# Kernel optimization log

Hardware: AMD Instinct MI355X
Metric: run time of the kernel (lower is better)

The kernel has to match this reference:

```python
import jax, jax.numpy as jnp
import numpy as np

EPS = 1e-5  # BatchNorm eps (inference mode, running_mean=0, running_var=1)

def conv3(x, w, b=None):
    y = jax.lax.conv_general_dilated(x, w, (1, 1), ((1, 1), (1, 1)),
                                     dimension_numbers=('NCHW', 'OIHW', 'NCHW'))
    if b is not None:
        y = y + b[None, :, None, None]
    return y

def bn(x, g):
    # g: [2, C] = (gamma, beta); eval-mode BN with running stats (0, 1)
    scale = (g[0] / jnp.sqrt(1.0 + EPS))[None, :, None, None]
    return x * scale + g[1][None, :, None, None]

def bcr(x, w, g, b=None):  # BasicConv2d: conv -> BN -> ReLU
    return jax.nn.relu(bn(conv3(x, w, b), g))

def setup_inputs() -> dict:
    key = jax.random.key(0)
    B, ch1, ch2, H, W = 2, 64, 128, 64, 64
    ks = jax.random.split(key, 16)
    w = lambda k, o, i: (jax.random.normal(k, (o, i, 3, 3), jnp.float32) * 0.05)
    g = lambda c: jnp.stack([jnp.ones((c,), jnp.float32), jnp.zeros((c,), jnp.float32)])
    return {
        'xs': jax.random.normal(ks[0], (B, ch1, H, W), jnp.float32),
        'xc': jax.random.normal(ks[1], (B, ch2, H, W), jnp.float32),
        'w_g1': w(ks[2], 32, ch1), 'g_g1': g(32),
        'w_g2': w(ks[3], 32, ch2), 'g_g2': g(32),
        'w_ls': w(ks[4], ch1, ch1 + 32), 'b_ls': jnp.zeros((ch1,), jnp.float32), 'g_ls': g(ch1),
        'w_lc': w(ks[5], ch2, ch2 + 32), 'b_lc': jnp.zeros((ch2,), jnp.float32), 'g_lc': g(ch2),
        'w_c1': w(ks[6], 32, ch1), 'g_c1': g(32),
        'w_c2': w(ks[7], 32, ch2), 'g_c2': g(32),
        'w_o1': w(ks[8], ch1, ch1), 'g_o1': g(ch1),
        'w_o2': w(ks[9], ch2, ch2), 'g_o2': g(ch2),
        'w_oa': w(ks[10], 1, 1), 'g_oa': g(1),
    }

def reference(xs, xc, w_g1, g_g1, w_g2, g_g2, w_ls, b_ls, g_ls,
              w_lc, b_lc, g_lc, w_c1, g_c1, w_c2, g_c2,
              w_o1, g_o1, w_o2, g_o2, w_oa, g_oa):
    B, ch1, H, W = xs.shape
    ch2 = xc.shape[1]
    N = H * W
    # global context: conv+BN+ReLU -> GAP (1x1) -> bilinear upsample from 1x1 == broadcast
    g_s = jnp.mean(bcr(xs, w_g1, g_g1), axis=(2, 3), keepdims=True)  # [B,32,1,1]
    g_c = jnp.mean(bcr(xc, w_g2, g_g2), axis=(2, 3), keepdims=True)
    gs = jnp.broadcast_to(g_s, (B, 32, H, W))
    gc = jnp.broadcast_to(g_c, (B, 32, H, W))
    xs1 = jax.nn.relu(bn(conv3(jnp.concatenate([gs, xs], axis=1), w_ls, b_ls), g_ls)) + xs
    xc1 = jax.nn.relu(bn(conv3(jnp.concatenate([gc, xc], axis=1), w_lc, b_lc), g_lc)) + xc
    # dual cross-spatial attention
    fs = bcr(xs1, w_c1, g_c1).reshape(B, 32, N)
    fc = bcr(xc1, w_c2, g_c2).reshape(B, 32, N)
    att = jnp.einsum('bcn,bcm->bnm', fs, fc)  # [B,N,N]
    sm_cols = jax.nn.softmax(att, axis=-2)    # softmax over n (rows)
    sm_rows = jax.nn.softmax(att, axis=-1)    # softmax over m
    outs = jnp.einsum('bcn,bnm->bcm', xs1.reshape(B, ch1, N), sm_cols).reshape(B, ch1, H, W)
    # xc_flat @ softmax(att^T, -2): (att^T).softmax(-2)[m,j] = sm_rows[j,m]
    outc = jnp.einsum('bcm,bjm->bcj', xc1.reshape(B, ch2, N), sm_rows).reshape(B, ch2, H, W)
    out_s = bcr(outs, w_o1, g_o1) + xs1
    out_c = bcr(outc, w_o2, g_o2) + xc1
    att2 = att + jnp.swapaxes(att, -1, -2)
    att3 = jax.nn.softmax(att2, axis=-2) + jnp.swapaxes(jax.nn.softmax(att2, axis=-1), -1, -2)
    att_map = bcr(att3[:, None], w_oa, g_oa)  # [B,1,N,N]
    return (att_map, out_s, out_c, g_s, g_c)
```

## Files before the change

### kernel.cpp

```cpp
#include <hip/hip_runtime.h>


#define LB __launch_bounds__(256)

constexpr float BN_SCALE = 0.99999500003749968f;
constexpr float NEG_BIG  = -3.402823466e38f;
constexpr float LOG2E    = 1.4426950408889634f;
constexpr float LN2      = 0.6931471805599453f;

typedef __attribute__((ext_vector_type(8))) short short8v;
typedef __attribute__((ext_vector_type(4))) float f32x4;

__device__ __forceinline__ ushort bf16rne(float f) {
    unsigned u = __float_as_uint(f);
    unsigned r = (u + 0x7FFFu + ((u >> 16) & 1u)) >> 16;
    return (ushort)r;
}

__device__ __forceinline__ void online_merge(float& mx, float& sm, float m2, float s2) {
    const float mn = fmaxf(mx, m2);
    sm = sm * __expf(mx - mn) + s2 * __expf(m2 - mn);
    mx = mn;
}

__global__ LB void transpose_bf(const float* __restrict__ in, ushort* __restrict__ outT,
                                int C, int HW)
{
    __shared__ float t[32][33];
    const int tid = threadIdx.x;
    const int tx = tid & 31, ty0 = tid >> 5;
    const int hw0 = blockIdx.x * 32, c0 = blockIdx.y * 32, b = blockIdx.z;
    #pragma unroll
    for (int i = 0; i < 4; ++i)
        t[ty0 + i * 8][tx] = in[((long)b * C + c0 + ty0 + i * 8) * HW + hw0 + tx];
    __syncthreads();
    #pragma unroll
    for (int i = 0; i < 4; ++i)
        outT[((long)b * HW + hw0 + ty0 + i * 8) * C + c0 + tx] =
            bf16rne(t[tx][ty0 + i * 8]);
}

template<int HASG, int OCB>
__global__ LB void conv3x3_mfma(
    const ushort* __restrict__ inT,
    const float* __restrict__ gconst,
    const float* __restrict__ w,
    const float* __restrict__ bias,
    const float* __restrict__ bn,
    const float* __restrict__ residual,
    float* __restrict__ out,
    ushort* __restrict__ outbf,
    ushort* __restrict__ outTbf,
    int Cg, int Cin, int Cout)
{
    constexpr int TILES = OCB / 16;
    constexpr int TPO = 256 / OCB;
    constexpr int J = 288 / TPO;
    __shared__ ushort ldsA[9][OCB][36];
    __shared__ float wg[OCB][10];
    const int tid = threadIdx.x;
    const int wv = tid >> 6, lane = tid & 63;
    const int fr = lane & 15, fg = lane >> 4;
    const int px0 = blockIdx.x * 64, ocb = blockIdx.y * OCB, b = blockIdx.z;
    const int Ct = Cg + Cin;
    const int p = px0 + wv * 16 + fr;
    const int y = p >> 6, x = p & 63;

    if (HASG) {
        for (int e = tid; e < OCB * 9; e += 256) {
            const int oc = e / 9, k = e % 9;
            float s = 0.f;
            for (int ic = 0; ic < Cg; ++ic)
                s += gconst[b * Cg + ic] * w[((long)(ocb + oc) * Ct + ic) * 9 + k];
            wg[oc][k] = s;
        }
    }

    int qv[9]; bool val[9];
    #pragma unroll
    for (int k = 0; k < 9; ++k) {
        const int yy = y + k / 3 - 1, xx = x + k % 3 - 1;
        val[k] = ((unsigned)yy < 64u) && ((unsigned)xx < 64u);
        qv[k] = val[k] ? (yy * 64 + xx) : 0;
    }

    f32x4 acc[TILES];
    #pragma unroll
    for (int t = 0; t < TILES; ++t) acc[t] = (f32x4){0.f, 0.f, 0.f, 0.f};
    const short8v bz = (short8v){0, 0, 0, 0, 0, 0, 0, 0};

    const int oc_st = tid / TPO, q = tid % TPO;
    const int base_ic = q * (J / 9);
    const ushort* inTb = inT + (long)b * 4096 * Cin + 8 * fg;

    const int NCH = Cin / 32;
    for (int c = 0; c < NCH; ++c) {
        __syncthreads();
        {
            const float* wp = w + (long)(ocb + oc_st) * Ct * 9
                              + (long)(Cg + c * 32) * 9 + q * J;
            #pragma unroll
            for (int j4 = 0; j4 < J; j4 += 4) {
                const float4 v4 = *(const float4*)&wp[j4];
                ldsA[(j4 + 0) % 9][oc_st][base_ic + (j4 + 0) / 9] = bf16rne(v4.x);
                ldsA[(j4 + 1) % 9][oc_st][base_ic + (j4 + 1) / 9] = bf16rne(v4.y);
                ldsA[(j4 + 2) % 9][oc_st][base_ic + (j4 + 2) / 9] = bf16rne(v4.z);
                ldsA[(j4 + 3) % 9][oc_st][base_ic + (j4 + 3) / 9] = bf16rne(v4.w);
            }
        }
        __syncthreads();
        const ushort* inc = inTb + c * 32;
        #pragma unroll
        for (int k = 0; k < 9; ++k) {
            const short8v bfrag = val[k] ? *(const short8v*)&inc[(long)qv[k] * Cin] : bz;
            #pragma unroll
            for (int t = 0; t < TILES; ++t) {
                const short8v afrag = *(const short8v*)&ldsA[k][t * 16 + fr][8 * fg];
                acc[t] = __builtin_amdgcn_mfma_f32_16x16x32_bf16(afrag, bfrag, acc[t], 0, 0, 0);
            }
        }
    }

    #pragma unroll
    for (int t = 0; t < TILES; ++t) {
        float v4[4];
        #pragma unroll
        for (int r = 0; r < 4; ++r) {
            const int ocl = t * 16 + fg * 4 + r;
            const int oc = ocb + ocl;
            float v = acc[t][r];
            if (bias) v += bias[oc];
            if (HASG) {
                #pragma unroll
                for (int k = 0; k < 9; ++k)
                    if (val[k]) v += wg[ocl][k];
            }
            v = fmaxf(fmaf(v, bn[oc] * BN_SCALE, bn[Cout + oc]), 0.f);
            const long oidx = ((long)(b * Cout + oc)) * 4096 + p;
            if (residual) v += residual[oidx];
            out[oidx] = v;
            if (outbf) outbf[oidx] = bf16rne(v);
            v4[r] = v;
        }
        if (outTbf) {
            ushort4 o;
            o.x = bf16rne(v4[0]); o.y = bf16rne(v4[1]);
            o.z = bf16rne(v4[2]); o.w = bf16rne(v4[3]);
            *(ushort4*)&outTbf[((long)(b * 4096 + p)) * Cout + ocb + t * 16 + fg * 4] = o;
        }
    }
}

__global__ LB void gap_kernel(const float* __restrict__ in,
                              float* __restrict__ o1, float* __restrict__ o2,
                              int C, int HW)
{
    const int c = blockIdx.x, b = blockIdx.y;
    const float* p = in + ((long)b * C + c) * HW;
    float s = 0.f;
    for (int i = threadIdx.x; i < HW; i += 256) s += p[i];
    #pragma unroll
    for (int off = 32; off; off >>= 1) s += __shfl_down(s, off);
    __shared__ float red[4];
    if ((threadIdx.x & 63) == 0) red[threadIdx.x >> 6] = s;
    __syncthreads();
    if (threadIdx.x == 0) {
        const float t = (red[0] + red[1] + red[2] + red[3]) / (float)HW;
        o1[b * C + c] = t;
        o2[b * C + c] = t;
    }
}

__global__ LB void att_gemm(const float* __restrict__ fs, const float* __restrict__ fc,
                            float* __restrict__ att, float* __restrict__ attT, int N)
{
    __shared__ float lfs[32][33];
    const int tid = threadIdx.x;
    const int m  = blockIdx.x * 256 + tid;
    const int n0 = blockIdx.y * 32;
    const int b  = blockIdx.z;
    for (int i = tid; i < 1024; i += 256) {
        const int c = i >> 5, nn = i & 31;
        lfs[c][nn] = fs[((long)b * 32 + c) * N + n0 + nn];
    }
    __syncthreads();
    float acc[32];
    #pragma unroll
    for (int i = 0; i < 32; ++i) acc[i] = 0.f;
    const float* fcp = fc + (long)b * 32 * N + m;
    #pragma unroll
    for (int c = 0; c < 32; ++c) {
        const float f = fcp[(long)c * N];
        #pragma unroll
        for (int nn = 0; nn < 32; ++nn) acc[nn] = fmaf(lfs[c][nn], f, acc[nn]);
    }
    float* op = att + ((long)b * N + n0) * N + m;
    #pragma unroll
    for (int nn = 0; nn < 32; ++nn) op[(long)nn * N] = acc[nn];
    float* opT = attT + ((long)b * N + m) * N + n0;
    #pragma unroll
    for (int q = 0; q < 8; ++q)
        *(float4*)&opT[q * 4] = make_float4(acc[q*4], acc[q*4+1], acc[q*4+2], acc[q*4+3]);
}

__global__ LB void tri_stats(const float* __restrict__ att, const float* __restrict__ attT,
                             float* __restrict__ McP, float* __restrict__ ScP,
                             float* __restrict__ MrP, float* __restrict__ SrP,
                             float* __restrict__ M2P, float* __restrict__ S2P, int N)
{
    __shared__ float lm[3][4][64], ls[3][4][64];
    const int c = threadIdx.x & 63, q = threadIdx.x >> 6;
    const int m = blockIdx.x * 64 + c;
    const int y = blockIdx.y, b = blockIdx.z;
    const long base = (long)b * N * N + ((long)y * 128 + q) * N + m;

    float av[32], tv[32];
    #pragma unroll
    for (int r = 0; r < 32; ++r) {
        const long off = base + (long)r * 4 * N;
        av[r] = att[off];
        tv[r] = attT[off];
    }
    float mc = av[0], mr = tv[0], m2 = av[0] + tv[0];
    #pragma unroll
    for (int r = 1; r < 32; ++r) {
        mc = fmaxf(mc, av[r]);
        mr = fmaxf(mr, tv[r]);
        m2 = fmaxf(m2, av[r] + tv[r]);
    }
    const float mcL = mc * LOG2E, mrL = mr * LOG2E, m2L = m2 * LOG2E;
    float sc = 0.f, sr = 0.f, s2 = 0.f;
    #pragma unroll
    for (int r = 0; r < 32; ++r) {
        sc += exp2f(fmaf(av[r], LOG2E, -mcL));
        sr += exp2f(fmaf(tv[r], LOG2E, -mrL));
        s2 += exp2f(fmaf(av[r] + tv[r], LOG2E, -m2L));
    }

    lm[0][q][c] = mc; ls[0][q][c] = sc;
    lm[1][q][c] = mr; ls[1][q][c] = sr;
    lm[2][q][c] = m2; ls[2][q][c] = s2;
    __syncthreads();
    if (q < 3) {
        float M = lm[q][0][c], S = ls[q][0][c];
        #pragma unroll
        for (int j = 1; j < 4; ++j) online_merge(M, S, lm[q][j][c], ls[q][j][c]);
        float* Pm = (q == 0) ? McP : ((q == 1) ? MrP : M2P);
        float* Ps = (q == 0) ? ScP : ((q == 1) ? SrP : S2P);
        Pm[((long)(b * 32 + y)) * N + m] = M;
        Ps[((long)(b * 32 + y)) * N + m] = S;
    }
}

__global__ LB void stats_comb32(const float* __restrict__ Mp, const float* __restrict__ Sp,
                                float* __restrict__ M, float* __restrict__ Sm,
                                float* __restrict__ C2L, int N)
{
    __shared__ float lm[4][64], ls[4][64];
    const int c = threadIdx.x & 63, q = threadIdx.x >> 6;
    const int n = blockIdx.x * 64 + c;
    const int b = blockIdx.y;
    float mx = NEG_BIG, sum = 0.f;
    #pragma unroll
    for (int j = 0; j < 8; ++j) {
        const int s = q * 8 + j;
        online_merge(mx, sum, Mp[((long)(b * 32 + s)) * N + n], Sp[((long)(b * 32 + s)) * N + n]);
    }
    lm[q][c] = mx; ls[q][c] = sum;
    __syncthreads();
    if (q == 0) {
        #pragma unroll
        for (int j = 1; j < 4; ++j) online_merge(mx, sum, lm[j][c], ls[j][c]);
        M[(long)b * N + n]  = mx;
        Sm[(long)b * N + n] = sum;
        if (C2L) C2L[(long)b * N + n] = (mx - LN2 + __logf(sum)) * LOG2E;
    }
}

template<int MROWS>
__global__ LB void sm_gemm_mfma(const ushort* __restrict__ Xbf,
                                const float* __restrict__ A,
                                const float* __restrict__ Mv,
                                float* __restrict__ p0, float* __restrict__ p1,
                                int N)
{
    constexpr int RT = MROWS / 32;
    constexpr int TPRA = 256 / MROWS;
    __shared__ ushort ldsA[MROWS][40];
    __shared__ ushort ldsB[32][40];

    const int tid = threadIdx.x;
    const int wave = tid >> 6, lane = tid & 63;
    const int col0 = blockIdx.x * 32;
    const int s = blockIdx.y, b = blockIdx.z;
    const int K0 = s * (N / 2);

    const int scol = tid >> 3, sq = tid & 7;
    const int ar = tid / TPRA;
    const int ak = (tid % TPRA) * (32 / TPRA);
    const int wct = wave & 1;
    const int wrh = wave >> 1;
    const int fr = lane & 15, fg = lane >> 4;

    f32x4 acc[RT];
    #pragma unroll
    for (int i = 0; i < RT; ++i) acc[i] = (f32x4){0.f, 0.f, 0.f, 0.f};

    const float* ab = A + ((long)b * N + col0) * N;
    const ushort* xb = Xbf + (long)b * MROWS * N;
    const float mvl = Mv[(long)b * N + col0 + scol] * LOG2E;

    for (int k0 = K0; k0 < K0 + N / 2; k0 += 32) {
        __syncthreads();
        #pragma unroll
        for (int j = 0; j < 32 / TPRA; j += 8) {
            const short8v av = *(const short8v*)&xb[(long)ar * N + k0 + ak + j];
            *(short8v*)&ldsA[ar][ak + j] = av;
        }
        const float4 v = *(const float4*)&ab[(long)scol * N + k0 + sq * 4];
        ushort4 bfv;
        bfv.x = bf16rne(exp2f(fmaf(v.x, LOG2E, -mvl)));
        bfv.y = bf16rne(exp2f(fmaf(v.y, LOG2E, -mvl)));
        bfv.z = bf16rne(exp2f(fmaf(v.z, LOG2E, -mvl)));
        bfv.w = bf16rne(exp2f(fmaf(v.w, LOG2E, -mvl)));
        *(ushort4*)&ldsB[scol][sq * 4] = bfv;
        __syncthreads();
        const short8v bfrag = *(const short8v*)&ldsB[wct * 16 + fr][8 * fg];
        #pragma unroll
        for (int rt = 0; rt < RT; ++rt) {
            const int row = wrh * (MROWS / 2) + rt * 16 + fr;
            const short8v afrag = *(const short8v*)&ldsA[row][8 * fg];
            acc[rt] = __builtin_amdgcn_mfma_f32_16x16x32_bf16(afrag, bfrag, acc[rt], 0, 0, 0);
        }
    }

    float* pp = (s == 0) ? p0 : p1;
    #pragma unroll
    for (int rt = 0; rt < RT; ++rt) {
        #pragma unroll
        for (int r = 0; r < 4; ++r) {
            const int row = wrh * (MROWS / 2) + rt * 16 + (lane >> 4) * 4 + r;
            const int col = col0 + wct * 16 + (lane & 15);
            pp[((long)b * MROWS + row) * N + col] = acc[rt][r];
        }
    }
}

template<int C>
__global__ LB void sm_reduce2(const float* __restrict__ p0, const float* __restrict__ p1,
                              const float* __restrict__ denom, float* __restrict__ outp, int N)
{
    const long idx = (long)blockIdx.x * 256 + threadIdx.x;
    const int m = (int)(idx & (long)(N - 1));
    const int b = (int)(idx / ((long)C * N));
    outp[idx] = (p0[idx] + p1[idx]) / denom[(long)b * N + m];
}

__global__ LB void attmap_conv(const float* __restrict__ att,
                               const float* __restrict__ attT,
                               const float* __restrict__ C2L,
                               const float* __restrict__ w, const float* __restrict__ g,
                               float* __restrict__ out, int N)
{
    __shared__ float tD[34][136];
    __shared__ float ldc[130];
    const int tid = threadIdx.x;
    const int x0 = (blockIdx.x & 31) * 128;
    const int y0 = (blockIdx.x >> 5) * 32;
    const int b = blockIdx.y;
    const float* ap = att + (long)b * N * N;
    const float* tp = attT + (long)b * N * N;
    const float* cp = C2L + (long)b * N;

    if (tid < 130) {
        const int xx = x0 + tid - 1;
        ldc[tid] = ((unsigned)xx < (unsigned)N) ? cp[xx] : 0.f;
    }
    __syncthreads();

    {
        const int xg = (tid & 31) * 4;
        const int rg = tid >> 5;
        #pragma unroll
        for (int i = 0; i < 5; ++i) {
            const int hy = rg + i * 8;
            if (hy < 34) {
                const int yy = y0 + hy - 1;
                float4 v = make_float4(0.f, 0.f, 0.f, 0.f);
                if ((unsigned)yy < (unsigned)N) {
                    const long off = (long)yy * N + x0 + xg;
                    const float4 a = *(const float4*)&ap[off];
                    const float4 t = *(const float4*)&tp[off];
                    v.x = exp2f(fmaf(a.x + t.x, LOG2E, -ldc[xg + 1]));
                    v.y = exp2f(fmaf(a.y + t.y, LOG2E, -ldc[xg + 2]));
                    v.z = exp2f(fmaf(a.z + t.z, LOG2E, -ldc[xg + 3]));
                    v.w = exp2f(fmaf(a.w + t.w, LOG2E, -ldc[xg + 4]));
                }
                *(float4*)&tD[hy][xg + 4] = v;
            }
        }
    }
    if (tid < 68) {
        const int c01 = tid & 1, hy = tid >> 1;
        const int col = c01 ? 132 : 3;
        const int xx = c01 ? (x0 + 128) : (x0 - 1);
        const int yy = y0 + hy - 1;
        float v = 0.f;
        if ((unsigned)yy < (unsigned)N && (unsigned)xx < (unsigned)N) {
            const long off = (long)yy * N + xx;
            v = exp2f(fmaf(ap[off] + tp[off], LOG2E, -ldc[c01 ? 129 : 0]));
        }
        tD[hy][col] = v;
    }
    __syncthreads();

    const float scale = g[0] * BN_SCALE, beta = g[1];
    const int tx2 = tid & 127, tyg = tid >> 7;
    float* ob = out + (long)b * N * N + (long)y0 * N + x0 + tx2;
    #pragma unroll
    for (int rr = 0; rr < 16; ++rr) {
        const int ly = tyg + rr * 2;
        float acc = 0.f;
        #pragma unroll
        for (int ky = 0; ky < 3; ++ky)
            #pragma unroll
            for (int kx = 0; kx < 3; ++kx)
                acc = fmaf(w[ky * 3 + kx], tD[ly + ky][tx2 + 3 + kx], acc);
        ob[(long)ly * N] = fmaxf(fmaf(acc, scale, beta), 0.f);
    }
}

extern "C" void kernel_launch(void* const* d_in, const int* in_sizes, int n_in,
                              void* d_out, int out_size, void* d_ws, size_t ws_size,
                              hipStream_t stream)
{
    const float* xs   = (const float*)d_in[0];
    const float* xc   = (const float*)d_in[1];
    const float* w_g1 = (const float*)d_in[2];
    const float* g_g1 = (const float*)d_in[3];
    const float* w_g2 = (const float*)d_in[4];
    const float* g_g2 = (const float*)d_in[5];
    const float* w_ls = (const float*)d_in[6];
    const float* b_ls = (const float*)d_in[7];
    const float* g_ls = (const float*)d_in[8];
    const float* w_lc = (const float*)d_in[9];
    const float* b_lc = (const float*)d_in[10];
    const float* g_lc = (const float*)d_in[11];
    const float* w_c1 = (const float*)d_in[12];
    const float* g_c1 = (const float*)d_in[13];
    const float* w_c2 = (const float*)d_in[14];
    const float* g_c2 = (const float*)d_in[15];
    const float* w_o1 = (const float*)d_in[16];
    const float* g_o1 = (const float*)d_in[17];
    const float* w_o2 = (const float*)d_in[18];
    const float* g_o2 = (const float*)d_in[19];
    const float* w_oa = (const float*)d_in[20];
    const float* g_oa = (const float*)d_in[21];

    const int B = 2, HW = 4096, N = 4096;

    float* ws = (float*)d_ws;
    float* xs1    = ws;
    float* xc1    = ws + 524288;
    float* fs     = ws + 1572864;
    float* fc     = ws + 1835008;
    float* t32    = ws + 2097152;
    float* McP    = ws + 1572864;
    float* ScP    = ws + 1835008;
    float* MrP    = ws + 2097152;
    float* SrP    = ws + 2359296;
    float* M2P    = ws + 2621440;
    float* S2P    = ws + 2883584;
    float* pg1    = ws + 1572864;
    float* outs_w = ws + 2359296;
    float* outc_w = ws + 2883584;
    float* gs_w   = ws + 3932160;
    float* gc_w   = ws + 3932224;
    float* Mc     = ws + 3932288;
    float* Sc     = ws + 3940480;
    float* Mr     = ws + 3948672;
    float* Sr     = ws + 3956864;
    float* M2     = ws + 3965056;
    float* S2     = ws + 3973248;
    float* C2L    = ws + 3981440;
    float* att    = ws + 4243584;
    float* attT   = ws + 37798016;

    float* out = (float*)d_out;
    float* out_attmap = out;
    ushort* xs1bf   = (ushort*)out;
    ushort* xc1bf   = (ushort*)(out + 262144);
    ushort* xcT     = (ushort*)(out + 786432);
    ushort* outcT   = (ushort*)(out + 786432);
    ushort* xsT     = (ushort*)(out + 1310720);
    ushort* outs_wT = (ushort*)(out + 1310720);
    ushort* xs1T    = (ushort*)(out + 1572864);
    ushort* xc1T    = (ushort*)(out + 1835008);
    float* out_s      = out + 33554432;
    float* out_c      = out + 34078720;
    float* out_gs     = out + 35127296;
    float* out_gc     = out + 35127360;
    float* pg0        = out + 33554432;

    const dim3 blk(256);

    transpose_bf<<<dim3(128, 2, B), blk, 0, stream>>>(xs, xsT, 64, HW);
    transpose_bf<<<dim3(128, 4, B), blk, 0, stream>>>(xc, xcT, 128, HW);
    conv3x3_mfma<0, 32><<<dim3(64, 1, B), blk, 0, stream>>>(xsT, nullptr, w_g1, nullptr, g_g1, nullptr, t32, nullptr, nullptr, 0, 64, 32);
    gap_kernel<<<dim3(32, B), blk, 0, stream>>>(t32, gs_w, out_gs, 32, HW);
    conv3x3_mfma<0, 32><<<dim3(64, 1, B), blk, 0, stream>>>(xcT, nullptr, w_g2, nullptr, g_g2, nullptr, t32, nullptr, nullptr, 0, 128, 32);
    gap_kernel<<<dim3(32, B), blk, 0, stream>>>(t32, gc_w, out_gc, 32, HW);
    conv3x3_mfma<1, 64><<<dim3(64, 1, B), blk, 0, stream>>>(xsT, gs_w, w_ls, b_ls, g_ls, xs, xs1, xs1bf, xs1T, 32, 64, 64);
    conv3x3_mfma<1, 64><<<dim3(64, 2, B), blk, 0, stream>>>(xcT, gc_w, w_lc, b_lc, g_lc, xc, xc1, xc1bf, xc1T, 32, 128, 128);
    conv3x3_mfma<0, 32><<<dim3(64, 1, B), blk, 0, stream>>>(xs1T, nullptr, w_c1, nullptr, g_c1, nullptr, fs, nullptr, nullptr, 0, 64, 32);
    conv3x3_mfma<0, 32><<<dim3(64, 1, B), blk, 0, stream>>>(xc1T, nullptr, w_c2, nullptr, g_c2, nullptr, fc, nullptr, nullptr, 0, 128, 32);
    att_gemm<<<dim3(16, 128, B), blk, 0, stream>>>(fs, fc, att, attT, N);
    tri_stats<<<dim3(64, 32, B), blk, 0, stream>>>(att, attT, McP, ScP, MrP, SrP, M2P, S2P, N);
    stats_comb32<<<dim3(64, B), blk, 0, stream>>>(McP, ScP, Mc, Sc, nullptr, N);
    stats_comb32<<<dim3(64, B), blk, 0, stream>>>(MrP, SrP, Mr, Sr, nullptr, N);
    stats_comb32<<<dim3(64, B), blk, 0, stream>>>(M2P, S2P, M2, S2, C2L, N);
    sm_gemm_mfma<128><<<dim3(128, 2, B), blk, 0, stream>>>(xc1bf, att, Mr, pg0, pg1, N);
    sm_reduce2<128><<<dim3((B * 128 * N) / 256), blk, 0, stream>>>(pg0, pg1, Sr, outc_w, N);
    transpose_bf<<<dim3(128, 4, B), blk, 0, stream>>>(outc_w, outcT, 128, HW);
    conv3x3_mfma<0, 64><<<dim3(64, 2, B), blk, 0, stream>>>(outcT, nullptr, w_o2, nullptr, g_o2, xc1, out_c, nullptr, nullptr, 0, 128, 128);
    sm_gemm_mfma<64><<<dim3(128, 2, B), blk, 0, stream>>>(xs1bf, attT, Mc, pg0, pg1, N);
    sm_reduce2<64><<<dim3((B * 64 * N) / 256), blk, 0, stream>>>(pg0, pg1, Sc, outs_w, N);
    transpose_bf<<<dim3(128, 2, B), blk, 0, stream>>>(outs_w, outs_wT, 64, HW);
    conv3x3_mfma<0, 64><<<dim3(64, 1, B), blk, 0, stream>>>(outs_wT, nullptr, w_o1, nullptr, g_o1, xs1, out_s, nullptr, nullptr, 0, 64, 64);
    attmap_conv<<<dim3(4096, B), blk, 0, stream>>>(att, attT, C2L, w_oa, g_oa, out_attmap, N);
}
```

Before: 580.0 us.

## Register-prefetch softmax-GEMM tiles, widen K step, and split K four ways

The softmax-weighted GEMM now loads the next K tile's attention and feature data into registers before computing the current tile, so global loads overlap the MFMA work. Each iteration covers 64 K elements instead of 32, which halves the number of barriers. The K dimension is split into four parts instead of two, doubling the grid. Partial results go to a new workspace buffer and are summed by a four-way reduce kernel. This costs more register use and twice the partial-sum traffic in the reduction.

```diff
diff --git a/kernel.cpp b/kernel.cpp
--- a/kernel.cpp
+++ b/kernel.cpp
@@ -281,79 +281,104 @@
 __global__ LB void sm_gemm_mfma(const ushort* __restrict__ Xbf,
                                 const float* __restrict__ A,
                                 const float* __restrict__ Mv,
-                                float* __restrict__ p0, float* __restrict__ p1,
+                                float* __restrict__ parts,
                                 int N)
 {
     constexpr int RT = MROWS / 32;
-    constexpr int TPRA = 256 / MROWS;
-    __shared__ ushort ldsA[MROWS][40];
-    __shared__ ushort ldsB[32][40];
+    constexpr int AR_SH = (MROWS == 128) ? 1 : 2;
+    constexpr int ALD = (MROWS == 128) ? 4 : 2;
+    __shared__ ushort ldsA[MROWS][80];
+    __shared__ ushort ldsB[32][80];
 
     const int tid = threadIdx.x;
     const int wave = tid >> 6, lane = tid & 63;
     const int col0 = blockIdx.x * 32;
     const int s = blockIdx.y, b = blockIdx.z;
-    const int K0 = s * (N / 2);
+    const int KLEN = N / 4, K0 = s * KLEN;
 
     const int scol = tid >> 3, sq = tid & 7;
-    const int ar = tid / TPRA;
-    const int ak = (tid % TPRA) * (32 / TPRA);
-    const int wct = wave & 1;
-    const int wrh = wave >> 1;
+    const int ar = tid >> AR_SH;
+    const int ak = (tid & ((1 << AR_SH) - 1)) * (ALD * 8);
+    const int wct = wave & 1, wrh = wave >> 1;
     const int fr = lane & 15, fg = lane >> 4;
 
     f32x4 acc[RT];
     #pragma unroll
     for (int i = 0; i < RT; ++i) acc[i] = (f32x4){0.f, 0.f, 0.f, 0.f};
 
-    const float* ab = A + ((long)b * N + col0) * N;
-    const ushort* xb = Xbf + (long)b * MROWS * N;
+    const float* ab = A + ((long)b * N + col0) * N + (long)scol * N + K0 + sq * 8;
+    const ushort* xb = Xbf + (long)b * MROWS * N + (long)ar * N + K0 + ak;
     const float mvl = Mv[(long)b * N + col0 + scol] * LOG2E;
 
-    for (int k0 = K0; k0 < K0 + N / 2; k0 += 32) {
+    float4 bv0 = *(const float4*)&ab[0];
+    float4 bv1 = *(const float4*)&ab[4];
+    short8v av[ALD];
+    #pragma unroll
+    for (int j = 0; j < ALD; ++j) av[j] = *(const short8v*)&xb[8 * j];
+
+    const int NIT = KLEN / 64;
+    for (int it = 0; it < NIT; ++it) {
         __syncthreads();
-        #pragma unroll
-        for (int j = 0; j < 32 / TPRA; j += 8) {
-            const short8v av = *(const short8v*)&xb[(long)ar * N + k0 + ak + j];
-            *(short8v*)&ldsA[ar][ak + j] = av;
-        }
-        const float4 v = *(const float4*)&ab[(long)scol * N + k0 + sq * 4];
-        ushort4 bfv;
-        bfv.x = bf16rne(exp2f(fmaf(v.x, LOG2E, -mvl)));
-        bfv.y = bf16rne(exp2f(fmaf(v.y, LOG2E, -mvl)));
-        bfv.z = bf16rne(exp2f(fmaf(v.z, LOG2E, -mvl)));
-        bfv.w = bf16rne(exp2f(fmaf(v.w, LOG2E, -mvl)));
-        *(ushort4*)&ldsB[scol][sq * 4] = bfv;
+        ushort4 o0, o1;
+        o0.x = bf16rne(exp2f(fmaf(bv0.x, LOG2E, -mvl)));
+        o0.y = bf16rne(exp2f(fmaf(bv0.y, LOG2E, -mvl)));
+        o0.z = bf16rne(exp2f(fmaf(bv0.z, LOG2E, -mvl)));
+        o0.w = bf16rne(exp2f(fmaf(bv0.w, LOG2E, -mvl)));
+        o1.x = bf16rne(exp2f(fmaf(bv1.x, LOG2E, -mvl)));
+        o1.y = bf16rne(exp2f(fmaf(bv1.y, LOG2E, -mvl)));
+        o1.z = bf16rne(exp2f(fmaf(bv1.z, LOG2E, -mvl)));
+        o1.w = bf16rne(exp2f(fmaf(bv1.w, LOG2E, -mvl)));
+        *(ushort4*)&ldsB[scol][sq * 8] = o0;
+        *(ushort4*)&ldsB[scol][sq * 8 + 4] = o1;
+        #pragma unroll
+        for (int j = 0; j < ALD; ++j) *(short8v*)&ldsA[ar][ak + 8 * j] = av[j];
         __syncthreads();
-        const short8v bfrag = *(const short8v*)&ldsB[wct * 16 + fr][8 * fg];
-        #pragma unroll
-        for (int rt = 0; rt < RT; ++rt) {
-            const int row = wrh * (MROWS / 2) + rt * 16 + fr;
-            const short8v afrag = *(const short8v*)&ldsA[row][8 * fg];
-            acc[rt] = __builtin_amdgcn_mfma_f32_16x16x32_bf16(afrag, bfrag, acc[rt], 0, 0, 0);
-        }
-    }
-
-    float* pp = (s == 0) ? p0 : p1;
+        if (it + 1 < NIT) {
+            const int kb = (it + 1) * 64;
+            bv0 = *(const float4*)&ab[kb];
+            bv1 = *(const float4*)&ab[kb + 4];
+            #pragma unroll
+            for (int j = 0; j < ALD; ++j)
+                av[j] = *(const short8v*)&xb[kb + 8 * j];
+        }
+        #pragma unroll
+        for (int kk = 0; kk < 2; ++kk) {
+            const short8v bfrag = *(const short8v*)&ldsB[wct * 16 + fr][32 * kk + 8 * fg];
+            #pragma unroll
+            for (int rt = 0; rt < RT; ++rt) {
+                const int row = wrh * (MROWS / 2) + rt * 16 + fr;
+                const short8v afrag = *(const short8v*)&ldsA[row][32 * kk + 8 * fg];
+                acc[rt] = __builtin_amdgcn_mfma_f32_16x16x32_bf16(afrag, bfrag, acc[rt], 0, 0, 0);
+            }
+        }
+    }
+
+    float* pp = parts + ((long)(s * 2 + b) * MROWS) * N;
     #pragma unroll
     for (int rt = 0; rt < RT; ++rt) {
         #pragma unroll
         for (int r = 0; r < 4; ++r) {
-            const int row = wrh * (MROWS / 2) + rt * 16 + (lane >> 4) * 4 + r;
-            const int col = col0 + wct * 16 + (lane & 15);
-            pp[((long)b * MROWS + row) * N + col] = acc[rt][r];
+            const int row = wrh * (MROWS / 2) + rt * 16 + fg * 4 + r;
+            const int col = col0 + wct * 16 + fr;
+            pp[(long)row * N + col] = acc[rt][r];
         }
     }
 }
 
 template<int C>
-__global__ LB void sm_reduce2(const float* __restrict__ p0, const float* __restrict__ p1,
+__global__ LB void sm_reduce4(const float* __restrict__ parts,
                               const float* __restrict__ denom, float* __restrict__ outp, int N)
 {
     const long idx = (long)blockIdx.x * 256 + threadIdx.x;
     const int m = (int)(idx & (long)(N - 1));
-    const int b = (int)(idx / ((long)C * N));
-    outp[idx] = (p0[idx] + p1[idx]) / denom[(long)b * N + m];
+    const long bc = idx >> 12;
+    const int c = (int)(bc & (C - 1));
+    const int b = (int)(bc / C);
+    float s = 0.f;
+    #pragma unroll
+    for (int ss = 0; ss < 4; ++ss)
+        s += parts[((long)(ss * 2 + b) * C + c) * N + m];
+    outp[idx] = s / denom[(long)b * N + m];
 }
 
 __global__ LB void attmap_conv(const float* __restrict__ att,
@@ -471,7 +496,6 @@
     float* SrP    = ws + 2359296;
     float* M2P    = ws + 2621440;
     float* S2P    = ws + 2883584;
-    float* pg1    = ws + 1572864;
     float* outs_w = ws + 2359296;
     float* outc_w = ws + 2883584;
     float* gs_w   = ws + 3932160;
@@ -485,6 +509,7 @@
     float* C2L    = ws + 3981440;
     float* att    = ws + 4243584;
     float* attT   = ws + 37798016;
+    float* pg     = ws + 71352448;
 
     float* out = (float*)d_out;
     float* out_attmap = out;
@@ -500,7 +525,6 @@
     float* out_c      = out + 34078720;
     float* out_gs     = out + 35127296;
     float* out_gc     = out + 35127360;
-    float* pg0        = out + 33554432;
 
     const dim3 blk(256);
 
@@ -519,12 +543,12 @@
     stats_comb32<<<dim3(64, B), blk, 0, stream>>>(McP, ScP, Mc, Sc, nullptr, N);
     stats_comb32<<<dim3(64, B), blk, 0, stream>>>(MrP, SrP, Mr, Sr, nullptr, N);
     stats_comb32<<<dim3(64, B), blk, 0, stream>>>(M2P, S2P, M2, S2, C2L, N);
-    sm_gemm_mfma<128><<<dim3(128, 2, B), blk, 0, stream>>>(xc1bf, att, Mr, pg0, pg1, N);
-    sm_reduce2<128><<<dim3((B * 128 * N) / 256), blk, 0, stream>>>(pg0, pg1, Sr, outc_w, N);
+    sm_gemm_mfma<128><<<dim3(128, 4, B), blk, 0, stream>>>(xc1bf, att, Mr, pg, N);
+    sm_reduce4<128><<<dim3((B * 128 * N) / 256), blk, 0, stream>>>(pg, Sr, outc_w, N);
     transpose_bf<<<dim3(128, 4, B), blk, 0, stream>>>(outc_w, outcT, 128, HW);
     conv3x3_mfma<0, 64><<<dim3(64, 2, B), blk, 0, stream>>>(outcT, nullptr, w_o2, nullptr, g_o2, xc1, out_c, nullptr, nullptr, 0, 128, 128);
-    sm_gemm_mfma<64><<<dim3(128, 2, B), blk, 0, stream>>>(xs1bf, attT, Mc, pg0, pg1, N);
-    sm_reduce2<64><<<dim3((B * 64 * N) / 256), blk, 0, stream>>>(pg0, pg1, Sc, outs_w, N);
+    sm_gemm_mfma<64><<<dim3(128, 4, B), blk, 0, stream>>>(xs1bf, attT, Mc, pg, N);
+    sm_reduce4<64><<<dim3((B * 64 * N) / 256), blk, 0, stream>>>(pg, Sc, outs_w, N);
     transpose_bf<<<dim3(128, 2, B), blk, 0, stream>>>(outs_w, outs_wT, 64, HW);
     conv3x3_mfma<0, 64><<<dim3(64, 1, B), blk, 0, stream>>>(outs_wT, nullptr, w_o1, nullptr, g_o1, xs1, out_s, nullptr, nullptr, 0, 64, 64);
     attmap_conv<<<dim3(4096, B), blk, 0, stream>>>(att, attT, C2L, w_oa, g_oa, out_attmap, N);
```

New measurement: 520.4 us. 10.3% less time.
